# Kernel tuning notes

Hardware: AMD Instinct MI355X
Metric: run time of the kernel (lower is better)

The kernel has to match this reference:

```python
import jax, jax.numpy as jnp
import numpy as np

D = 16      # stroke_embedding_dim
H = 2       # num_heads
DH = D // H # head dim = 8
HID = 32    # hidden_dim
OUT = 32    # output_dim
N = 250000  # num edge nodes
F = 500000  # num faces
E = 4       # edges per face


def setup_inputs() -> dict:
    key = jax.random.key(0)
    ks = jax.random.split(key, 10)
    s = 1.0 / np.sqrt(D)
    return {
        "node_embed": jax.random.normal(ks[0], (1, N, D), dtype=jnp.float32),
        "face_edge_ids": jax.random.randint(ks[1], (F, E), 0, N),
        # nn.MultiheadAttention in_proj (packed q,k,v) and out_proj, stored [in, out]
        "w_in": jax.random.uniform(ks[2], (D, 3 * D), jnp.float32, -s, s),
        "b_in": jnp.zeros((3 * D,), jnp.float32),
        "w_out": jax.random.uniform(ks[3], (D, D), jnp.float32, -s, s),
        "b_out": jnp.zeros((D,), jnp.float32),
        # fc: Linear(16 -> 32), fc_output: Linear(32 -> 32)
        "fc_w": jax.random.uniform(ks[4], (D, HID), jnp.float32, -s, s),
        "fc_b": jax.random.uniform(ks[5], (HID,), jnp.float32, -s, s),
        "fco_w": jax.random.uniform(ks[6], (HID, OUT), jnp.float32, -1 / np.sqrt(HID), 1 / np.sqrt(HID)),
        "fco_b": jax.random.uniform(ks[7], (OUT,), jnp.float32, -1 / np.sqrt(HID), 1 / np.sqrt(HID)),
    }


def reference(node_embed, face_edge_ids, w_in, b_in, w_out, b_out, fc_w, fc_b, fco_w, fco_b):
    # Gather per-face edge embeddings: [F, E, D]
    x = node_embed[0][face_edge_ids]
    # Packed qkv projection
    qkv = x @ w_in + b_in                                  # [F, E, 3D]
    q, k, v = jnp.split(qkv, 3, axis=-1)
    def heads(t):
        return t.reshape(F, E, H, DH).transpose(0, 2, 1, 3)  # [F, H, E, DH]
    q, k, v = heads(q), heads(k), heads(v)
    scores = jnp.einsum("fhqd,fhkd->fhqk", q, k) / np.sqrt(DH)
    attn = jax.nn.softmax(scores, axis=-1)
    o = jnp.einsum("fhqk,fhkd->fhqd", attn, v)             # [F, H, E, DH]
    o = o.transpose(0, 2, 1, 3).reshape(F, E, D)
    attn_out = o @ w_out + b_out                           # [F, E, D]
    h = jax.nn.relu(attn_out @ fc_w + fc_b)                # [F, E, HID]
    pooled = h.mean(axis=1)                                # [F, HID]
    out = pooled @ fco_w + fco_b                           # [F, OUT]
    return out[None]                                       # [1, F, OUT]
```

## Files before the change

### kernel.cpp

```cpp
#include <hip/hip_runtime.h>
#include <stdint.h>


typedef _Float16 v2h __attribute__((ext_vector_type(2)));
typedef __fp16 h4 __attribute__((ext_vector_type(4)));
typedef float f32x4 __attribute__((ext_vector_type(4)));
typedef uint32_t u32x2 __attribute__((ext_vector_type(2)));

#define DPP_ROT2 0x4E
#define DPP_XOR1 0xB1

template<int CTRL>
static __device__ __forceinline__ float dppf(float x) {
    return __builtin_bit_cast(float,
        __builtin_amdgcn_mov_dpp(__builtin_bit_cast(int, x), CTRL, 0xF, 0xF, true));
}

static __device__ __forceinline__ v2h pkh(float a, float b) {
    v2h r; r.x = (_Float16)a; r.y = (_Float16)b; return r;
}
static __device__ __forceinline__ v2h pkrtz(float a, float b) {
#if __has_builtin(__builtin_amdgcn_cvt_pkrtz)
    return __builtin_bit_cast(v2h, __builtin_amdgcn_cvt_pkrtz(a, b));
#else
    return pkh(a, b);
#endif
}
static __device__ __forceinline__ uint32_t bcu(v2h h) {
    return __builtin_bit_cast(uint32_t, h);
}
static __device__ __forceinline__ h4 mkh4(uint32_t lo, uint32_t hi) {
    u32x2 t; t.x = lo; t.y = hi; return __builtin_bit_cast(h4, t);
}
static __device__ __forceinline__ h4 ld2h(const uint32_t* p) {
    u32x2 t; t.x = p[0]; t.y = p[1]; return __builtin_bit_cast(h4, t);
}
static __device__ __forceinline__ f32x4 mfma16(h4 a, h4 b, f32x4 c) {
    return __builtin_amdgcn_mfma_f32_16x16x16f16(a, b, c, 0, 0, 0);
}
static __device__ __forceinline__ h4 packC(f32x4 c) {
    return mkh4(bcu(pkrtz(c[0], c[1])), bcu(pkrtz(c[2], c[3])));
}
static __device__ __forceinline__ h4 selh(bool keep, h4 x) {
    u32x2 t = __builtin_bit_cast(u32x2, x);
    u32x2 r; r.x = keep ? t.x : 0u; r.y = keep ? t.y : 0u;
    return __builtin_bit_cast(h4, r);
}

__global__ void fold_w(const float* __restrict__ w_in,
                       const float* __restrict__ w_out,
                       const float* __restrict__ b_out,
                       const float* __restrict__ fc_w,
                       const float* __restrict__ fc_b,
                       const float* __restrict__ fco_w,
                       uint32_t* __restrict__ wsu) {
    const int tid = threadIdx.x;
    if (blockIdx.x == 0) {
        if (tid < 384) {
            const int T = tid >> 7, r = tid & 127, l = r >> 1, d = r & 1;
            const int o = 16 * T + (l & 15), k0 = 4 * (l >> 4) + 2 * d;
            wsu[tid] = bcu(pkh(w_in[k0 * 48 + o], w_in[(k0 + 1) * 48 + o]));
        } else if (tid < 640) {
            const int i = tid - 384, b = i >> 7, r = i & 127, l = r >> 1, d = r & 1;
            const int c = 16 * b + (l & 15), k0 = 4 * (l >> 4) + 2 * d;
            float a0 = 0.f, a1 = 0.f;
#pragma unroll
            for (int e = 0; e < 16; ++e) {
                a0 = fmaf(w_out[k0 * 16 + e],       fc_w[e * 32 + c], a0);
                a1 = fmaf(w_out[(k0 + 1) * 16 + e], fc_w[e * 32 + c], a1);
            }
            wsu[tid] = bcu(pkh(a0, a1));
        }
    } else {
        if (tid < 32) {
            float acc = fc_b[tid];
#pragma unroll
            for (int e = 0; e < 16; ++e)
                acc = fmaf(b_out[e], fc_w[e * 32 + tid], acc);
            reinterpret_cast<float*>(wsu)[640 + tid] = acc;
        } else if (tid < 544) {
            const int i = tid - 32;
            const int kt = i >> 8, n = (i >> 7) & 1, r = i & 127, l = r >> 1, d = r & 1;
            const int col = 16 * n + (l & 15), k0 = 16 * kt + 4 * (l >> 4) + 2 * d;
            wsu[672 + i] = bcu(pkh(fco_w[k0 * 32 + col] * 0.25f,
                                   fco_w[(k0 + 1) * 32 + col] * 0.25f));
        }
    }
}

__launch_bounds__(256, 4)
__global__ void face_net(const float* __restrict__ node,
                         const int*   __restrict__ fids,
                         const float* __restrict__ b_in,
                         const uint32_t* __restrict__ wsu,
                         const float* __restrict__ fco_b,
                         float* __restrict__ out, int F) {
    const int l   = threadIdx.x & 63;
    const int wid = threadIdx.x >> 6;
    const int token_base = blockIdx.x * 256 + wid * 64;
    const int total = 4 * F;
    if (token_base >= total) return;
    const int c0 = l & 15, g2 = l >> 4;

    h4 X[4];
#pragma unroll
    for (int a = 0; a < 4; ++a) {
        int tok = token_base + 16 * a + c0;
        tok = tok < total ? tok : total - 1;
        const int nid = fids[tok];
        const float4 xv = *reinterpret_cast<const float4*>(
            node + (size_t)nid * 16 + g2 * 4);
        X[a] = mkh4(bcu(pkrtz(xv.x, xv.y)), bcu(pkrtz(xv.z, xv.w)));
    }

    const h4 WqT  = ld2h(wsu + 0   + l * 2);
    const h4 WkT  = ld2h(wsu + 128 + l * 2);
    const h4 WvB  = ld2h(wsu + 256 + l * 2);
    const h4 EhA0 = ld2h(wsu + 384 + l * 2);
    const h4 EhA1 = ld2h(wsu + 512 + l * 2);
    const h4 Ef00 = ld2h(wsu + 672 + 0 * 128 + l * 2);
    const h4 Ef01 = ld2h(wsu + 672 + 1 * 128 + l * 2);
    const h4 Ef10 = ld2h(wsu + 672 + 2 * 128 + l * 2);
    const h4 Ef11 = ld2h(wsu + 672 + 3 * 128 + l * 2);

    const float4 bq4 = *reinterpret_cast<const float4*>(b_in + 4 * g2);
    const float  bv  = b_in[32 + c0];
    const float* b1f = reinterpret_cast<const float*>(wsu) + 640;
    const float4 b10 = *reinterpret_cast<const float4*>(b1f + 4 * g2);
    const float4 b11 = *reinterpret_cast<const float4*>(b1f + 16 + 4 * g2);
    const float4 fb0 = *reinterpret_cast<const float4*>(fco_b + 4 * g2);
    const float4 fb1 = *reinterpret_cast<const float4*>(fco_b + 16 + 4 * g2);

    const bool scoreH0 = (g2 < 2);
    const bool pvH0    = (c0 < 8);
    const bool valid   = (g2 == (c0 >> 2));
    const int fbase = token_base >> 2;
    const float C = 0.51006974841f;
    const f32x4 zz = {0.f, 0.f, 0.f, 0.f};

#pragma unroll
    for (int a = 0; a < 4; ++a) {
        f32x4 cq = {bq4.x, bq4.y, bq4.z, bq4.w};
        f32x4 cv = {bv, bv, bv, bv};
        const f32x4 Dq = mfma16(WqT, X[a], cq);
        const f32x4 Dk = mfma16(WkT, X[a], zz);
        const f32x4 Dv = mfma16(X[a], WvB, cv);
        const h4 qB = packC(Dq);
        const h4 kA = packC(Dk);
        const h4 vA = packC(Dv);

        const f32x4 S0 = mfma16(selh(scoreH0,  kA), qB, zz);
        const f32x4 S1 = mfma16(selh(!scoreH0, kA), qB, zz);

        const float e00 = __builtin_amdgcn_exp2f(S0[0] * C);
        const float e01 = __builtin_amdgcn_exp2f(S0[1] * C);
        const float e02 = __builtin_amdgcn_exp2f(S0[2] * C);
        const float e03 = __builtin_amdgcn_exp2f(S0[3] * C);
        const float e10 = __builtin_amdgcn_exp2f(S1[0] * C);
        const float e11 = __builtin_amdgcn_exp2f(S1[1] * C);
        const float e12 = __builtin_amdgcn_exp2f(S1[2] * C);
        const float e13 = __builtin_amdgcn_exp2f(S1[3] * C);
        const float r0 = __builtin_amdgcn_rcpf((e00 + e01) + (e02 + e03));
        const float r1 = __builtin_amdgcn_rcpf((e10 + e11) + (e12 + e13));
        const h4 PB0 = selh(valid, mkh4(bcu(pkrtz(e00 * r0, e01 * r0)),
                                        bcu(pkrtz(e02 * r0, e03 * r0))));
        const h4 PB1 = selh(valid, mkh4(bcu(pkrtz(e10 * r1, e11 * r1)),
                                        bcu(pkrtz(e12 * r1, e13 * r1))));

        f32x4 Ot = mfma16(selh(pvH0,  vA), PB0, zz);
        Ot       = mfma16(selh(!pvH0, vA), PB1, Ot);
        const h4 hB = packC(Ot);

        f32x4 ch0 = {b10.x, b10.y, b10.z, b10.w};
        f32x4 ch1 = {b11.x, b11.y, b11.z, b11.w};
        const f32x4 H0 = mfma16(EhA0, hB, ch0);
        const f32x4 H1 = mfma16(EhA1, hB, ch1);
        float pool[8];
#pragma unroll
        for (int r = 0; r < 4; ++r) {
            float x0 = fmaxf(H0[r], 0.f);
            float s0 = x0 + dppf<DPP_XOR1>(x0); s0 = s0 + dppf<DPP_ROT2>(s0);
            pool[r] = s0;
            float x1 = fmaxf(H1[r], 0.f);
            float s1 = x1 + dppf<DPP_XOR1>(x1); s1 = s1 + dppf<DPP_ROT2>(s1);
            pool[4 + r] = s1;
        }
        const h4 pB0 = mkh4(bcu(pkrtz(pool[0], pool[1])),
                            bcu(pkrtz(pool[2], pool[3])));
        const h4 pB1 = mkh4(bcu(pkrtz(pool[4], pool[5])),
                            bcu(pkrtz(pool[6], pool[7])));

        f32x4 cf0 = {fb0.x, fb0.y, fb0.z, fb0.w};
        f32x4 cf1 = {fb1.x, fb1.y, fb1.z, fb1.w};
        const f32x4 O0 = mfma16(Ef10, pB1, mfma16(Ef00, pB0, cf0));
        const f32x4 O1 = mfma16(Ef11, pB1, mfma16(Ef01, pB0, cf1));

        if ((c0 & 3) == 0) {
            const int face = fbase + 4 * a + (c0 >> 2);
            float* ob = out + (size_t)face * 32 + 4 * g2;
            *reinterpret_cast<float4*>(ob)      = make_float4(O0[0], O0[1], O0[2], O0[3]);
            *reinterpret_cast<float4*>(ob + 16) = make_float4(O1[0], O1[1], O1[2], O1[3]);
        }
    }
}

extern "C" void kernel_launch(void* const* d_in, const int* in_sizes, int n_in,
                              void* d_out, int out_size, void* d_ws, size_t ws_size,
                              hipStream_t stream) {
    const float* node  = (const float*)d_in[0];
    const int*   fids  = (const int*)  d_in[1];
    const float* w_in  = (const float*)d_in[2];
    const float* b_in  = (const float*)d_in[3];
    const float* w_out = (const float*)d_in[4];
    const float* b_out = (const float*)d_in[5];
    const float* fc_w  = (const float*)d_in[6];
    const float* fc_b  = (const float*)d_in[7];
    const float* fco_w = (const float*)d_in[8];
    const float* fco_b = (const float*)d_in[9];
    float* out = (float*)d_out;
    uint32_t* wsu = (uint32_t*)d_ws;
    const int F = in_sizes[1] / 4;

    hipLaunchKernelGGL(fold_w, dim3(2), dim3(640), 0, stream,
                       w_in, w_out, b_out, fc_w, fc_b, fco_w, wsu);
    const int threads = F * 4;
    const int blocks = (threads + 255) / 256;
    hipLaunchKernelGGL(face_net, dim3(blocks), dim3(256), 0, stream,
                       node, fids, b_in, wsu, fco_b, out, F);
}
```

Measured before the change: 135.7 us.

## Fold mean-pool into output MFMA by swapping operands and summing per-lane rows

Replaces the DPP cross-lane reduction for mean pooling with an operand-swapped MFMA whose per-lane 4-row output is summed locally, so each lane writes one output column of one face. It also adds a face bounds check and raises launch_bounds min blocks from 4 to 8. The aim is to drop the DPP shuffles and the lane-masked float4 stores. In exchange, stores become scalar per lane, and the tighter register budget could cause spills.

Measured after the change: 160.2 us. 1.18x slower.

```diff
diff --git a/kernel.cpp b/kernel.cpp
--- a/kernel.cpp
+++ b/kernel.cpp
@@ -6,15 +6,6 @@
 typedef __fp16 h4 __attribute__((ext_vector_type(4)));
 typedef float f32x4 __attribute__((ext_vector_type(4)));
 typedef uint32_t u32x2 __attribute__((ext_vector_type(2)));
-
-#define DPP_ROT2 0x4E
-#define DPP_XOR1 0xB1
-
-template<int CTRL>
-static __device__ __forceinline__ float dppf(float x) {
-    return __builtin_bit_cast(float,
-        __builtin_amdgcn_mov_dpp(__builtin_bit_cast(int, x), CTRL, 0xF, 0xF, true));
-}
 
 static __device__ __forceinline__ v2h pkh(float a, float b) {
     v2h r; r.x = (_Float16)a; r.y = (_Float16)b; return r;
@@ -40,6 +31,10 @@
 }
 static __device__ __forceinline__ h4 packC(f32x4 c) {
     return mkh4(bcu(pkrtz(c[0], c[1])), bcu(pkrtz(c[2], c[3])));
+}
+static __device__ __forceinline__ h4 packCrelu(f32x4 c) {
+    return mkh4(bcu(pkrtz(fmaxf(c[0], 0.f), fmaxf(c[1], 0.f))),
+                bcu(pkrtz(fmaxf(c[2], 0.f), fmaxf(c[3], 0.f))));
 }
 static __device__ __forceinline__ h4 selh(bool keep, h4 x) {
     u32x2 t = __builtin_bit_cast(u32x2, x);
@@ -88,7 +83,7 @@
     }
 }
 
-__launch_bounds__(256, 4)
+__launch_bounds__(256, 8)
 __global__ void face_net(const float* __restrict__ node,
                          const int*   __restrict__ fids,
                          const float* __restrict__ b_in,
@@ -128,8 +123,8 @@
     const float* b1f = reinterpret_cast<const float*>(wsu) + 640;
     const float4 b10 = *reinterpret_cast<const float4*>(b1f + 4 * g2);
     const float4 b11 = *reinterpret_cast<const float4*>(b1f + 16 + 4 * g2);
-    const float4 fb0 = *reinterpret_cast<const float4*>(fco_b + 4 * g2);
-    const float4 fb1 = *reinterpret_cast<const float4*>(fco_b + 16 + 4 * g2);
+    const float fb0s = fco_b[c0];
+    const float fb1s = fco_b[16 + c0];
 
     const bool scoreH0 = (g2 < 2);
     const bool pvH0    = (c0 < 8);
@@ -175,31 +170,20 @@
         f32x4 ch1 = {b11.x, b11.y, b11.z, b11.w};
         const f32x4 H0 = mfma16(EhA0, hB, ch0);
         const f32x4 H1 = mfma16(EhA1, hB, ch1);
-        float pool[8];
-#pragma unroll
-        for (int r = 0; r < 4; ++r) {
-            float x0 = fmaxf(H0[r], 0.f);
-            float s0 = x0 + dppf<DPP_XOR1>(x0); s0 = s0 + dppf<DPP_ROT2>(s0);
-            pool[r] = s0;
-            float x1 = fmaxf(H1[r], 0.f);
-            float s1 = x1 + dppf<DPP_XOR1>(x1); s1 = s1 + dppf<DPP_ROT2>(s1);
-            pool[4 + r] = s1;
-        }
-        const h4 pB0 = mkh4(bcu(pkrtz(pool[0], pool[1])),
-                            bcu(pkrtz(pool[2], pool[3])));
-        const h4 pB1 = mkh4(bcu(pkrtz(pool[4], pool[5])),
-                            bcu(pkrtz(pool[6], pool[7])));
-
-        f32x4 cf0 = {fb0.x, fb0.y, fb0.z, fb0.w};
-        f32x4 cf1 = {fb1.x, fb1.y, fb1.z, fb1.w};
-        const f32x4 O0 = mfma16(Ef10, pB1, mfma16(Ef00, pB0, cf0));
-        const f32x4 O1 = mfma16(Ef11, pB1, mfma16(Ef01, pB0, cf1));
-
-        if ((c0 & 3) == 0) {
-            const int face = fbase + 4 * a + (c0 >> 2);
-            float* ob = out + (size_t)face * 32 + 4 * g2;
-            *reinterpret_cast<float4*>(ob)      = make_float4(O0[0], O0[1], O0[2], O0[3]);
-            *reinterpret_cast<float4*>(ob + 16) = make_float4(O1[0], O1[1], O1[2], O1[3]);
+
+        const h4 AH0 = packCrelu(H0);
+        const h4 AH1 = packCrelu(H1);
+
+        const f32x4 O0 = mfma16(AH1, Ef10, mfma16(AH0, Ef00, zz));
+        const f32x4 O1 = mfma16(AH1, Ef11, mfma16(AH0, Ef01, zz));
+        const float o0 = ((O0[0] + O0[1]) + (O0[2] + O0[3])) + fb0s;
+        const float o1 = ((O1[0] + O1[1]) + (O1[2] + O1[3])) + fb1s;
+
+        const int face = fbase + 4 * a + g2;
+        if (face < F) {
+            float* ob = out + (size_t)face * 32;
+            ob[c0]      = o0;
+            ob[16 + c0] = o1;
         }
     }
 }
```
